# Kernel optimization log

Hardware: AMD Instinct MI355X
Metric: run time of the kernel (lower is better)

The kernel has to match this reference:

```python
import jax, jax.numpy as jnp
import numpy as np

B, S, INPUT_DIM = 8, 512, 64
D_MODEL, NUM_LAYERS, OUTPUT_DIM = 512, 4, 10
D_INNER, D_STATE, D_CONV, DT_RANK = 2 * D_MODEL, 16, 4, 32
GRID_SIZE, SPLINE_K = 5, 3
N_COEFF = GRID_SIZE + SPLINE_K  # 8
_H = 2.0 / GRID_SIZE
GRID = jnp.linspace(-1.0 - SPLINE_K * _H, 1.0 + SPLINE_K * _H, GRID_SIZE + 2 * SPLINE_K + 1)


def b_splines(x):
    # x: (..., in) -> (..., in, N_COEFF) via Cox-de Boor recursion on fixed GRID
    x = x[..., None]
    b = ((x >= GRID[:-1]) & (x < GRID[1:])).astype(x.dtype)
    for p in range(1, SPLINE_K + 1):
        left = (x - GRID[:-(p + 1)]) / (GRID[p:-1] - GRID[:-(p + 1)])
        right = (GRID[p + 1:] - x) / (GRID[p + 1:] - GRID[1:-p])
        b = left * b[..., :-1] + right * b[..., 1:]
    return b


def kan(x, base_w, spline_w):
    # efficient-KAN: silu base path + per-edge spline path
    return jax.nn.silu(x) @ base_w.T + jnp.einsum('...ik,oik->...o', b_splines(x), spline_w)


def layernorm(x, g, b):
    m = jnp.mean(x, -1, keepdims=True)
    v = jnp.var(x, -1, keepdims=True)
    return (x - m) / jnp.sqrt(v + 1e-5) * g + b


def liquid_proj(x, Win, Wrec, b, tau):
    # liquid time-constant RNN: h' = (tanh(Wx + Uh + b) - h) / tau
    pre = x @ Win  # (B,S,H)
    tau_pos = jax.nn.softplus(tau) + 0.1
    def step(h, p):
        act = jnp.tanh(p + h @ Wrec + b)
        h = h + (act - h) / tau_pos
        return h, h
    h0 = jnp.zeros((x.shape[0], Win.shape[1]), x.dtype)
    hT, hs = jax.lax.scan(step, h0, pre.transpose(1, 0, 2))
    return hs.transpose(1, 0, 2), hT


def mamba_block(x, in_proj_w, conv_w, conv_b, x_proj_w, dt_proj_w, dt_proj_b, A_log, Dp, out_proj_w):
    Bb, Ss, _ = x.shape
    xz = x @ in_proj_w.T                       # (B,S,2*di)
    xm, z = jnp.split(xz, 2, axis=-1)
    # causal depthwise conv1d with kernel D_CONV
    xp = jnp.pad(xm, ((0, 0), (D_CONV - 1, 0), (0, 0)))
    xm = sum(xp[:, k:k + Ss, :] * conv_w[:, k] for k in range(D_CONV)) + conv_b
    xm = jax.nn.silu(xm)
    x_dbl = xm @ x_proj_w.T                    # (B,S,dt_rank+2n)
    dt, Bc, Cc = jnp.split(x_dbl, [DT_RANK, DT_RANK + D_STATE], axis=-1)
    dt = jax.nn.softplus(dt @ dt_proj_w.T + dt_proj_b)   # (B,S,di)
    A = -jnp.exp(A_log)                        # (di,n)
    dA = jnp.exp(dt[..., None] * A)            # (B,S,di,n)
    dBu = dt[..., None] * Bc[:, :, None, :] * xm[..., None]
    def step(h, inp):
        a, bu, c = inp
        h = a * h + bu
        return h, jnp.einsum('bdn,bn->bd', h, c)
    h0 = jnp.zeros((Bb, D_INNER, D_STATE), x.dtype)
    _, ys = jax.lax.scan(step, h0, (dA.transpose(1, 0, 2, 3), dBu.transpose(1, 0, 2, 3), Cc.transpose(1, 0, 2)))
    y = ys.transpose(1, 0, 2) + Dp * xm
    y = y * jax.nn.silu(z)
    return y @ out_proj_w.T


def forward(x, lq_Win, lq_Wrec, lq_b, lq_tau, ln_g, ln_b, in_proj_w, conv_w, conv_b,
            x_proj_w, dt_proj_w, dt_proj_b, A_log, Dp, out_proj_w,
            kan_base_w, kan_spline_w, fn_g, fn_b, cls_base_w, cls_spline_w):
    x, _ = liquid_proj(x, lq_Win, lq_Wrec, lq_b, lq_tau)
    for l in range(NUM_LAYERS):
        residual = x
        xn = layernorm(x, ln_g[l], ln_b[l])
        xm = mamba_block(xn, in_proj_w[l], conv_w[l], conv_b[l], x_proj_w[l],
                         dt_proj_w[l], dt_proj_b[l], A_log[l], Dp[l], out_proj_w[l])
        x = residual + kan(xm, kan_base_w[l], kan_spline_w[l])
    x = layernorm(x, fn_g, fn_b)
    return kan(x.mean(axis=1), cls_base_w, cls_spline_w)


def setup_inputs():
    key = jax.random.key(0)
    ks = jax.random.split(key, 12)
    n = lambda k, shape, s: jax.random.normal(k, shape, jnp.float32) * s
    return {
        "x": n(ks[0], (B, S, INPUT_DIM), 1.0),
        "lq_Win": n(ks[1], (INPUT_DIM, D_MODEL), INPUT_DIM ** -0.5),
        "lq_Wrec": n(ks[2], (D_MODEL, D_MODEL), D_MODEL ** -0.5),
        "lq_b": jnp.zeros((D_MODEL,), jnp.float32),
        "lq_tau": jnp.ones((D_MODEL,), jnp.float32),
        "ln_g": jnp.ones((NUM_LAYERS, D_MODEL), jnp.float32),
        "ln_b": jnp.zeros((NUM_LAYERS, D_MODEL), jnp.float32),
        "in_proj_w": n(ks[3], (NUM_LAYERS, 2 * D_INNER, D_MODEL), D_MODEL ** -0.5),
        "conv_w": n(ks[4], (NUM_LAYERS, D_INNER, D_CONV), D_CONV ** -0.5),
        "conv_b": jnp.zeros((NUM_LAYERS, D_INNER), jnp.float32),
        "x_proj_w": n(ks[5], (NUM_LAYERS, DT_RANK + 2 * D_STATE, D_INNER), D_INNER ** -0.5),
        "dt_proj_w": n(ks[6], (NUM_LAYERS, D_INNER, DT_RANK), DT_RANK ** -0.5),
        "dt_proj_b": jnp.full((NUM_LAYERS, D_INNER), float(np.log(np.expm1(0.01))), jnp.float32),
        "A_log": jnp.log(jnp.broadcast_to(jnp.arange(1, D_STATE + 1, dtype=jnp.float32), (NUM_LAYERS, D_INNER, D_STATE))),
        "Dp": jnp.ones((NUM_LAYERS, D_INNER), jnp.float32),
        "out_proj_w": n(ks[7], (NUM_LAYERS, D_MODEL, D_INNER), D_INNER ** -0.5),
        "kan_base_w": n(ks[8], (NUM_LAYERS, D_MODEL, D_MODEL), D_MODEL ** -0.5),
        "kan_spline_w": n(ks[9], (NUM_LAYERS, D_MODEL, D_MODEL, N_COEFF), 0.1 * D_MODEL ** -0.5),
        "fn_g": jnp.ones((D_MODEL,), jnp.float32),
        "fn_b": jnp.zeros((D_MODEL,), jnp.float32),
        "cls_base_w": n(ks[10], (OUTPUT_DIM, D_MODEL), D_MODEL ** -0.5),
        "cls_spline_w": n(ks[11], (OUTPUT_DIM, D_MODEL, N_COEFF), 0.1 * D_MODEL ** -0.5),
    }


def reference(x, lq_Win, lq_Wrec, lq_b, lq_tau, ln_g, ln_b, in_proj_w, conv_w, conv_b,
              x_proj_w, dt_proj_w, dt_proj_b, A_log, Dp, out_proj_w,
              kan_base_w, kan_spline_w, fn_g, fn_b, cls_base_w, cls_spline_w):
    return forward(x, lq_Win, lq_Wrec, lq_b, lq_tau, ln_g, ln_b, in_proj_w, conv_w, conv_b,
                   x_proj_w, dt_proj_w, dt_proj_b, A_log, Dp, out_proj_w,
                   kan_base_w, kan_spline_w, fn_g, fn_b, cls_base_w, cls_spline_w)
```

## Files before the change

### kernel.cpp

```cpp
#include <hip/hip_runtime.h>
#include <hip/hip_bf16.h>
#include <cmath>

#define DEV __device__ __forceinline__

constexpr int B_ = 8, S_ = 512, IN_ = 64, D_ = 512, L_ = 4;
constexpr int DI_ = 1024, DCONV_ = 4, DTR_ = 32;
constexpr int ROWS = B_ * S_;

constexpr size_t MB = 1ull << 20;
constexpr size_t OFF_X    = 0;
constexpr size_t OFF_XN   = OFF_X   + 8*MB;
constexpr size_t OFF_XZ   = OFF_XN  + 8*MB;
constexpr size_t OFF_XM   = OFF_XZ  + 32*MB;
constexpr size_t OFF_DT   = OFF_XM  + 16*MB;
constexpr size_t OFF_XDBL = OFF_DT  + 16*MB;
constexpr size_t OFF_YG   = OFF_XDBL+ 1*MB;
constexpr size_t OFF_MO   = OFF_YG  + 16*MB;
constexpr size_t OFF_WINT = OFF_MO  + 8*MB;
constexpr size_t OFF_MEAN = OFF_WINT+ 128*1024;
constexpr size_t OFF_HBUF = OFF_MEAN+ 16*1024;
constexpr size_t OFF_FLG  = OFF_HBUF+ 32*1024;
constexpr size_t OFF_W16  = OFF_FLG + 64*1024;
constexpr size_t OFF_BASIS= OFF_XZ;

constexpr size_t W_IP = 0;
constexpr size_t W_OP = 1048576;
constexpr size_t W_KB = 1572864;
constexpr size_t W_KS = 1835008;
constexpr size_t W_XP = 3932160;
constexpr size_t W_DT = 3997696;
constexpr size_t W_PER_LAYER = 4030464;

DEV float siluf(float x){ return x / (1.f + __expf(-x)); }
DEV float softplusf(float x){ return fmaxf(x, 0.f) + log1pf(__expf(-fabsf(x))); }
DEV unsigned short f2h(float f){ return __builtin_bit_cast(unsigned short, (_Float16)f); }
DEV float h2f(unsigned short u){ return (float)__builtin_bit_cast(_Float16, u); }
DEV int pk2(float a, float b){ return (int)((unsigned)f2h(a) | ((unsigned)f2h(b) << 16)); }

typedef _Float16 half8 __attribute__((ext_vector_type(8)));
typedef float f32x4 __attribute__((ext_vector_type(4)));

DEV void bspline8(float x, float* bb){
  const float h = 0.4f, g0 = -2.2f;
  float b0[11];
#pragma unroll
  for (int j = 0; j < 11; ++j){
    float gj  = g0 + h * j;
    float gj1 = g0 + h * (j + 1);
    b0[j] = (x >= gj && x < gj1) ? 1.f : 0.f;
  }
#pragma unroll
  for (int p = 1; p <= 3; ++p){
    float inv = 1.f / (h * p);
#pragma unroll
    for (int j = 0; j + p < 11; ++j){
      float gj  = g0 + h * j;
      float gip = g0 + h * (j + p + 1);
      b0[j] = (x - gj) * inv * b0[j] + (gip - x) * inv * b0[j + 1];
    }
  }
#pragma unroll
  for (int c = 0; c < 8; ++c) bb[c] = b0[c];
}

__global__ __launch_bounds__(256)
void conv_w16(const float* __restrict__ ip, const float* __restrict__ op,
              const float* __restrict__ kb, const float* __restrict__ ks,
              const float* __restrict__ xp, const float* __restrict__ dt,
              unsigned short* __restrict__ w16)
{
  int blk = blockIdx.x, tid = threadIdx.x;
  const float* src; size_t doff; int sb;
  if      (blk < 512) { src = ip; doff = W_IP; sb = blk; }
  else if (blk < 768) { src = op; doff = W_OP; sb = blk - 512; }
  else if (blk < 896) { src = kb; doff = W_KB; sb = blk - 768; }
  else if (blk < 1920){ src = ks; doff = W_KS; sb = blk - 896; }
  else if (blk < 1952){ src = xp; doff = W_XP; sb = blk - 1920; }
  else                { src = dt; doff = W_DT; sb = blk - 1952; }
  size_t e = (size_t)sb * 2048 + tid * 8;
  float4 a = *(const float4*)(src + e), b = *(const float4*)(src + e + 4);
  int4 v = { pk2(a.x,a.y), pk2(a.z,a.w), pk2(b.x,b.y), pk2(b.z,b.w) };
  *(int4*)&w16[doff + e] = v;
}

template<bool SILU_A, int EPI>
__global__ __launch_bounds__(256)
void gemm_nt(const float* __restrict__ A, int lda,
             const float* __restrict__ W, int ldw,
             float* __restrict__ C, int ldc,
             const float* __restrict__ bias, int K)
{
  __shared__ float As[16][68];
  __shared__ float Ws[16][68];
  const int tid = threadIdx.x;
  const int m0 = blockIdx.y * 64, n0 = blockIdx.x * 64;
  const int lr = tid >> 2, lc = (tid & 3) * 4;
  const float* Ap = A + (size_t)(m0 + lr) * lda + lc;
  const float* Wp = W + (size_t)(n0 + lr) * ldw + lc;
  const int tx = tid & 15, ty = tid >> 4;
  float acc[4][4] = {};
  for (int k0 = 0; k0 < K; k0 += 16){
    float4 a = *(const float4*)(Ap + k0);
    float4 w = *(const float4*)(Wp + k0);
    if (SILU_A){ a.x = siluf(a.x); a.y = siluf(a.y); a.z = siluf(a.z); a.w = siluf(a.w); }
    __syncthreads();
    As[lc+0][lr] = a.x; As[lc+1][lr] = a.y; As[lc+2][lr] = a.z; As[lc+3][lr] = a.w;
    Ws[lc+0][lr] = w.x; Ws[lc+1][lr] = w.y; Ws[lc+2][lr] = w.z; Ws[lc+3][lr] = w.w;
    __syncthreads();
#pragma unroll
    for (int k = 0; k < 16; ++k){
      float4 av = *(const float4*)&As[k][ty*4];
      float4 wv = *(const float4*)&Ws[k][tx*4];
      acc[0][0] += av.x*wv.x; acc[0][1] += av.x*wv.y; acc[0][2] += av.x*wv.z; acc[0][3] += av.x*wv.w;
      acc[1][0] += av.y*wv.x; acc[1][1] += av.y*wv.y; acc[1][2] += av.y*wv.z; acc[1][3] += av.y*wv.w;
      acc[2][0] += av.z*wv.x; acc[2][1] += av.z*wv.y; acc[2][2] += av.z*wv.z; acc[2][3] += av.z*wv.w;
      acc[3][0] += av.w*wv.x; acc[3][1] += av.w*wv.y; acc[3][2] += av.w*wv.z; acc[3][3] += av.w*wv.w;
    }
  }
#pragma unroll
  for (int i = 0; i < 4; ++i){
    float* Crow = C + (size_t)(m0 + ty*4 + i) * ldc + n0 + tx*4;
    float4 r = {acc[i][0], acc[i][1], acc[i][2], acc[i][3]};
    *(float4*)Crow = r;
  }
}


template<int AMODE>
DEV void stage_a(const void* Av, int lda, int m0, int sr, int k0, int sh,
                 int4& av0, int4& av1)
{
  if (AMODE == 0){
    const unsigned short* ag = (const unsigned short*)Av + (size_t)(m0 + sr) * lda + k0 + sh*16;
    av0 = *(const int4*)ag; av1 = *(const int4*)(ag + 8);
  } else {
    const float* ag = (const float*)Av + (size_t)(m0 + sr) * lda + k0 + sh*16;
    float4 a0 = *(const float4*)ag,     a1 = *(const float4*)(ag+4);
    float4 a2 = *(const float4*)(ag+8), a3 = *(const float4*)(ag+12);
    if (AMODE == 2){
      a0.x=siluf(a0.x); a0.y=siluf(a0.y); a0.z=siluf(a0.z); a0.w=siluf(a0.w);
      a1.x=siluf(a1.x); a1.y=siluf(a1.y); a1.z=siluf(a1.z); a1.w=siluf(a1.w);
      a2.x=siluf(a2.x); a2.y=siluf(a2.y); a2.z=siluf(a2.z); a2.w=siluf(a2.w);
      a3.x=siluf(a3.x); a3.y=siluf(a3.y); a3.z=siluf(a3.z); a3.w=siluf(a3.w);
    }
    av0 = (int4){ pk2(a0.x,a0.y), pk2(a0.z,a0.w), pk2(a1.x,a1.y), pk2(a1.z,a1.w) };
    av1 = (int4){ pk2(a2.x,a2.y), pk2(a2.z,a2.w), pk2(a3.x,a3.y), pk2(a3.z,a3.w) };
  }
}

template<int EPI>
DEV void epi_store(void* Cv, size_t off, float v, const float* bias, int col)
{
  if (EPI == 0)      ((float*)Cv)[off] = v;
  else if (EPI == 1) ((float*)Cv)[off] += v;
  else if (EPI == 2) ((float*)Cv)[off] = softplusf(v + bias[col]);
  else               ((unsigned short*)Cv)[off] = f2h(v);
}

template<int AMODE, int EPI>
__global__ __launch_bounds__(256)
void gemm_h128(const void* __restrict__ Av, int lda,
               const unsigned short* __restrict__ W,
               void* __restrict__ Cv, int ldc,
               const float* __restrict__ bias, int K)
{
  __shared__ unsigned short As[128*40];
  __shared__ unsigned short Bs[128*40];
  const int tid = threadIdx.x;
  const int m0 = blockIdx.y * 128, n0 = blockIdx.x * 128;
  const int wid = tid >> 6, lane = tid & 63;
  const int wm = (wid & 1) * 64, wn = (wid >> 1) * 64;
  const int fr = lane & 15, fk = lane >> 4;
  const int sr = tid >> 1, sh = tid & 1;

  f32x4 acc[4][4];
#pragma unroll
  for (int i = 0; i < 4; ++i)
#pragma unroll
    for (int j = 0; j < 4; ++j)
#pragma unroll
      for (int r = 0; r < 4; ++r) acc[i][j][r] = 0.f;

  for (int k0 = 0; k0 < K; k0 += 32){
    int4 av0, av1;
    stage_a<AMODE>(Av, lda, m0, sr, k0, sh, av0, av1);
    const unsigned short* wg = W + (size_t)(n0 + sr) * K + k0 + sh*16;
    int4 bv0 = *(const int4*)wg, bv1 = *(const int4*)(wg + 8);
    __syncthreads();
    *(int4*)&As[sr*40 + sh*16]     = av0;
    *(int4*)&As[sr*40 + sh*16 + 8] = av1;
    *(int4*)&Bs[sr*40 + sh*16]     = bv0;
    *(int4*)&Bs[sr*40 + sh*16 + 8] = bv1;
    __syncthreads();
    half8 a[4], b[4];
#pragma unroll
    for (int i = 0; i < 4; ++i) a[i] = *(const half8*)&As[(wm + i*16 + fr)*40 + fk*8];
#pragma unroll
    for (int j = 0; j < 4; ++j) b[j] = *(const half8*)&Bs[(wn + j*16 + fr)*40 + fk*8];
#pragma unroll
    for (int i = 0; i < 4; ++i)
#pragma unroll
      for (int j = 0; j < 4; ++j)
        acc[i][j] = __builtin_amdgcn_mfma_f32_16x16x32_f16(a[i], b[j], acc[i][j], 0, 0, 0);
  }
#pragma unroll
  for (int i = 0; i < 4; ++i)
#pragma unroll
    for (int j = 0; j < 4; ++j){
      int col = n0 + wn + j*16 + fr;
#pragma unroll
      for (int r = 0; r < 4; ++r){
        int row = m0 + wm + i*16 + fk*4 + r;
        epi_store<EPI>(Cv, (size_t)row * ldc + col, acc[i][j][r], bias, col);
      }
    }
}

template<int AMODE, int EPI>
__global__ __launch_bounds__(256)
void gemm_h64(const void* __restrict__ Av, int lda,
              const unsigned short* __restrict__ W,
              void* __restrict__ Cv, int ldc,
              const float* __restrict__ bias, int K)
{
  __shared__ unsigned short As[128*40];
  __shared__ unsigned short Bs[64*40];
  const int tid = threadIdx.x;
  const int m0 = blockIdx.y * 128, n0 = blockIdx.x * 64;
  const int wid = tid >> 6, lane = tid & 63;
  const int fr = lane & 15, fk = lane >> 4;
  const int sr = tid >> 1, sh = tid & 1;
  const int br = tid >> 2, bq = tid & 3;

  f32x4 acc[2][4];
#pragma unroll
  for (int i = 0; i < 2; ++i)
#pragma unroll
    for (int j = 0; j < 4; ++j)
#pragma unroll
      for (int r = 0; r < 4; ++r) acc[i][j][r] = 0.f;

  for (int k0 = 0; k0 < K; k0 += 32){
    int4 av0, av1;
    stage_a<AMODE>(Av, lda, m0, sr, k0, sh, av0, av1);
    const unsigned short* wg = W + (size_t)(n0 + br) * K + k0 + bq*8;
    int4 bv0 = *(const int4*)wg;
    __syncthreads();
    *(int4*)&As[sr*40 + sh*16]     = av0;
    *(int4*)&As[sr*40 + sh*16 + 8] = av1;
    *(int4*)&Bs[br*40 + bq*8]      = bv0;
    __syncthreads();
    half8 a[2], b[4];
#pragma unroll
    for (int i = 0; i < 2; ++i) a[i] = *(const half8*)&As[(wid*32 + i*16 + fr)*40 + fk*8];
#pragma unroll
    for (int j = 0; j < 4; ++j) b[j] = *(const half8*)&Bs[(j*16 + fr)*40 + fk*8];
#pragma unroll
    for (int i = 0; i < 2; ++i)
#pragma unroll
      for (int j = 0; j < 4; ++j)
        acc[i][j] = __builtin_amdgcn_mfma_f32_16x16x32_f16(a[i], b[j], acc[i][j], 0, 0, 0);
  }
#pragma unroll
  for (int i = 0; i < 2; ++i)
#pragma unroll
    for (int j = 0; j < 4; ++j){
      int col = n0 + j*16 + fr;
#pragma unroll
      for (int r = 0; r < 4; ++r){
        int row = m0 + wid*32 + i*16 + fk*4 + r;
        epi_store<EPI>(Cv, (size_t)row * ldc + col, acc[i][j][r], bias, col);
      }
    }
}

__global__ __launch_bounds__(256)
void transpose_win(const float* __restrict__ Win, float* __restrict__ WinT)
{
  int idx = blockIdx.x * 256 + threadIdx.x;
  int n = idx >> 6, k = idx & 63;
  WinT[idx] = Win[(size_t)k * 512 + n];
}

__global__ __launch_bounds__(512)
void liquid_scan3(const float* __restrict__ pre, const float* __restrict__ Wrec,
                  const float* __restrict__ bias, const float* __restrict__ tau,
                  float* __restrict__ xout, float* __restrict__ hbuf,
                  unsigned* __restrict__ flags)
{
  __shared__ float Wl[32800];
  __shared__ float hl[544];
  __shared__ float hnew[64];
  const int tid = threadIdx.x;
  const int bid = blockIdx.x;
  const int slice = bid >> 3, b = bid & 7;
  for (int idx = tid; idx < 512*16; idx += 512){
    int k = idx >> 4, c4 = (idx & 15) * 4;
    float4 w = *(const float4*)(Wrec + (size_t)k*512 + slice*64 + c4);
    *(float4*)&Wl[k*64 + c4 + (k>>6)*4] = w;
  }
  hl[tid + (tid>>6)*4] = 0.f;
  const int o = tid >> 3, kl = tid & 7;
  const int og = slice*64 + o;
  const float tauinv = 1.f / (softplusf(tau[og]) + 0.1f);
  const float bo = bias[og];
  float hold = 0.f;
  const float* preb = pre + (size_t)b * S_ * 512;
  float* xb = xout + (size_t)b * S_ * 512;
  float* hb0 = hbuf + (size_t)b * 512;
  unsigned* bflags = flags + b*8*16;
  unsigned* myflag = bflags + slice*16;
  const int kbase = kl * 64;
  const float* wp = &Wl[(size_t)kbase*64 + o + kl*4];
  __syncthreads();
  for (int t = 0; t < S_; ++t){
    float prev = (kl == 0) ? preb[(size_t)t*512 + og] : 0.f;
    float hreg[64];
#pragma unroll
    for (int j4 = 0; j4 < 16; ++j4)
      *(float4*)&hreg[j4*4] = *(const float4*)&hl[kbase + kl*4 + j4*4];
    float s = 0.f;
#pragma unroll
    for (int j = 0; j < 64; ++j)
      s += hreg[j] * wp[(size_t)j * 64];
    s += __shfl_xor(s, 1);
    s += __shfl_xor(s, 2);
    s += __shfl_xor(s, 4);
    if (kl == 0){
      float act = tanhf(s + prev + bo);
      hold += (act - hold) * tauinv;
      xb[(size_t)t*512 + og] = hold;
      hnew[o] = hold;
    }
    __syncthreads();
    if (tid < 64)
      __hip_atomic_store(hb0 + (t&1)*4096 + slice*64 + tid, hnew[tid],
                         __ATOMIC_RELAXED, __HIP_MEMORY_SCOPE_AGENT);
    if (tid == 0){
      asm volatile("s_waitcnt vmcnt(0)" ::: "memory");
      __hip_atomic_store(myflag, (unsigned)(t+1),
                         __ATOMIC_RELAXED, __HIP_MEMORY_SCOPE_AGENT);
    }
    if (tid < 8){
      while (__hip_atomic_load(bflags + tid*16, __ATOMIC_RELAXED,
                               __HIP_MEMORY_SCOPE_AGENT) < (unsigned)(t+1)) { }
    }
    __syncthreads();
    float hv = __hip_atomic_load(hb0 + (t&1)*4096 + tid,
                                 __ATOMIC_RELAXED, __HIP_MEMORY_SCOPE_AGENT);
    hl[tid + (tid>>6)*4] = hv;
    __syncthreads();
  }
}

__global__ __launch_bounds__(256)
void conv_silu(const unsigned short* __restrict__ xz, const float* __restrict__ cw,
               const float* __restrict__ cb, unsigned short* __restrict__ xm)
{
  int idx = blockIdx.x * 256 + threadIdx.x;
  int d = idx & 1023;
  int bs = idx >> 10;
  int t = bs & 511;
  const unsigned short* p = xz + (size_t)bs * 2048 + d;
  float4 w = *(const float4*)(cw + d*4);
  float acc = cb[d] + w.w * h2f(p[0]);
  if (t >= 1) acc += w.z * h2f(p[-2048]);
  if (t >= 2) acc += w.y * h2f(p[-2*2048]);
  if (t >= 3) acc += w.x * h2f(p[-3*2048]);
  xm[idx] = f2h(siluf(acc));
}

__global__ __launch_bounds__(256)
void mamba_scan2(const float* __restrict__ dt, const unsigned short* __restrict__ xm,
                 const float* __restrict__ xdbl, const unsigned short* __restrict__ xz,
                 const float* __restrict__ A_log, const float* __restrict__ Dp,
                 unsigned short* __restrict__ yg)
{
  const int tid = threadIdx.x;
  const int wave = tid >> 6, lane = tid & 63;
  const int ch = lane >> 3, sub = lane & 7;
  const int d = blockIdx.x * 32 + wave * 8 + ch;
  const int b = blockIdx.y;
  float2 al = *(const float2*)(A_log + (size_t)d*16 + sub*2);
  const float A0 = -__expf(al.x), A1 = -__expf(al.y);
  const float Dv = Dp[d];
  float h0 = 0.f, h1 = 0.f;
  const size_t rb = (size_t)b * S_;
  const float* dtp = dt + rb*1024 + d;
  const unsigned short* xmp = xm + rb*1024 + d;
  const unsigned short* zp  = xz + rb*2048 + 1024 + d;
  const float* bcp = xdbl + rb*64 + 32 + sub*2;
  const float* ccp = xdbl + rb*64 + 48 + sub*2;
  unsigned short* yp = yg + rb*1024 + d;
#pragma unroll 2
  for (int t = 0; t < S_; ++t){
    float dtv = dtp[(size_t)t*1024];
    float xv  = h2f(xmp[(size_t)t*1024]);
    float2 B2 = *(const float2*)(bcp + (size_t)t*64);
    float2 C2 = *(const float2*)(ccp + (size_t)t*64);
    float cbu = dtv * xv;
    h0 = __expf(dtv * A0) * h0 + cbu * B2.x;
    h1 = __expf(dtv * A1) * h1 + cbu * B2.y;
    float y = h0 * C2.x + h1 * C2.y;
    y += __shfl_xor(y, 1);
    y += __shfl_xor(y, 2);
    y += __shfl_xor(y, 4);
    if (sub == 0){
      float zv = h2f(zp[(size_t)t*2048]);
      yp[(size_t)t*1024] = f2h((y + Dv * xv) * siluf(zv));
    }
  }
}

template<bool H>
__global__ __launch_bounds__(256)
void layernorm_k(const float* __restrict__ x, const float* __restrict__ g,
                 const float* __restrict__ b, void* __restrict__ y)
{
  __shared__ float red[8];
  const int row = blockIdx.x, tid = threadIdx.x;
  const float* xr = x + (size_t)row * 512;
  float2 v = *(const float2*)(xr + tid*2);
  float s = v.x + v.y;
#pragma unroll
  for (int o = 32; o; o >>= 1) s += __shfl_xor(s, o);
  if ((tid & 63) == 0) red[tid >> 6] = s;
  __syncthreads();
  float mean = (red[0] + red[1] + red[2] + red[3]) * (1.f/512.f);
  float dx = v.x - mean, dy = v.y - mean;
  float q = dx*dx + dy*dy;
#pragma unroll
  for (int o = 32; o; o >>= 1) q += __shfl_xor(q, o);
  if ((tid & 63) == 0) red[4 + (tid >> 6)] = q;
  __syncthreads();
  float var = (red[4] + red[5] + red[6] + red[7]) * (1.f/512.f);
  float rstd = rsqrtf(var + 1e-5f);
  float2 gg = *(const float2*)(g + tid*2);
  float2 bb = *(const float2*)(b + tid*2);
  float ox = dx*rstd*gg.x + bb.x;
  float oy = dy*rstd*gg.y + bb.y;
  if (H){
    unsigned* yr = (unsigned*)y + (size_t)row*256 + tid;
    *yr = (unsigned)f2h(ox) | ((unsigned)f2h(oy) << 16);
  } else {
    float2 o2 = {ox, oy};
    *(float2*)((float*)y + (size_t)row*512 + tid*2) = o2;
  }
}

__global__ __launch_bounds__(256)
void bspline_kernel(const float* __restrict__ xin, unsigned short* __restrict__ basis)
{
  int idx = blockIdx.x * 256 + threadIdx.x;
  float x = xin[idx];
  float bb[8];
  bspline8(x, bb);
  int4 v = { pk2(bb[0],bb[1]), pk2(bb[2],bb[3]), pk2(bb[4],bb[5]), pk2(bb[6],bb[7]) };
  *(int4*)(basis + (size_t)idx * 8) = v;
}

__global__ __launch_bounds__(512)
void mean_over_s(const float* __restrict__ x, float* __restrict__ out)
{
  int b = blockIdx.x, d = threadIdx.x;
  const float* p = x + (size_t)b*S_*512 + d;
  float s = 0.f;
  for (int t = 0; t < S_; ++t) s += p[(size_t)t*512];
  out[b*512 + d] = s * (1.f/512.f);
}

__global__ __launch_bounds__(64)
void cls_kan(const float* __restrict__ xmean, const float* __restrict__ bw,
             const float* __restrict__ sw, float* __restrict__ out)
{
  int o = blockIdx.x % 10, b = blockIdx.x / 10;
  int lane = threadIdx.x;
  float acc = 0.f;
  for (int i = lane; i < 512; i += 64){
    float xv = xmean[b*512 + i];
    acc += siluf(xv) * bw[o*512 + i];
    float bb[8]; bspline8(xv, bb);
    const float* sp = sw + ((size_t)(o*512 + i)) * 8;
#pragma unroll
    for (int c = 0; c < 8; ++c) acc += bb[c] * sp[c];
  }
#pragma unroll
  for (int off = 32; off; off >>= 1) acc += __shfl_xor(acc, off);
  if (lane == 0) out[b*10 + o] = acc;
}

extern "C" void kernel_launch(void* const* d_in, const int* in_sizes, int n_in,
                              void* d_out, int out_size, void* d_ws, size_t ws_size,
                              hipStream_t stream)
{
  const float* x_in    = (const float*)d_in[0];
  const float* lq_Win  = (const float*)d_in[1];
  const float* lq_Wrec = (const float*)d_in[2];
  const float* lq_b    = (const float*)d_in[3];
  const float* lq_tau  = (const float*)d_in[4];
  const float* ln_g    = (const float*)d_in[5];
  const float* ln_bi   = (const float*)d_in[6];
  const float* in_proj = (const float*)d_in[7];
  const float* conv_w  = (const float*)d_in[8];
  const float* conv_b  = (const float*)d_in[9];
  const float* x_proj  = (const float*)d_in[10];
  const float* dt_w    = (const float*)d_in[11];
  const float* dt_b    = (const float*)d_in[12];
  const float* A_log   = (const float*)d_in[13];
  const float* Dp      = (const float*)d_in[14];
  const float* out_w   = (const float*)d_in[15];
  const float* kb_w    = (const float*)d_in[16];
  const float* ks_w    = (const float*)d_in[17];
  const float* fn_g    = (const float*)d_in[18];
  const float* fn_b    = (const float*)d_in[19];
  const float* cb_w    = (const float*)d_in[20];
  const float* cs_w    = (const float*)d_in[21];
  float* out = (float*)d_out;

  char* ws = (char*)d_ws;
  float* xcur  = (float*)(ws + OFF_X);
  float* xn32  = (float*)(ws + OFF_XN);
  unsigned short* xn16 = (unsigned short*)(ws + OFF_XN);
  unsigned short* xz16 = (unsigned short*)(ws + OFF_XZ);
  unsigned short* xm16 = (unsigned short*)(ws + OFF_XM);
  float* dtb   = (float*)(ws + OFF_DT);
  float* xdbl  = (float*)(ws + OFF_XDBL);
  unsigned short* yg16 = (unsigned short*)(ws + OFF_YG);
  float* mo    = (float*)(ws + OFF_MO);
  float* wint  = (float*)(ws + OFF_WINT);
  float* xmean = (float*)(ws + OFF_MEAN);
  float* hbufp = (float*)(ws + OFF_HBUF);
  unsigned* flgp = (unsigned*)(ws + OFF_FLG);
  unsigned short* w16 = (unsigned short*)(ws + OFF_W16);
  unsigned short* basis = (unsigned short*)(ws + OFF_BASIS);

  transpose_win<<<128, 256, 0, stream>>>(lq_Win, wint);
  gemm_nt<false,0><<<dim3(D_/64, ROWS/64), 256, 0, stream>>>(x_in, IN_, wint, IN_, xn32, D_, nullptr, IN_);
  hipMemsetAsync(flgp, 0, 8*8*16*sizeof(unsigned), stream);
  liquid_scan3<<<64, 512, 0, stream>>>(xn32, lq_Wrec, lq_b, lq_tau, xcur, hbufp, flgp);

  for (int l = 0; l < L_; ++l){
    conv_w16<<<1968, 256, 0, stream>>>(
        in_proj + (size_t)l*2*DI_*D_, out_w + (size_t)l*D_*DI_,
        kb_w + (size_t)l*D_*D_, ks_w + (size_t)l*D_*D_*8,
        x_proj + (size_t)l*64*DI_, dt_w + (size_t)l*DI_*DTR_,
        w16 + (size_t)l*W_PER_LAYER);
  }

  for (int l = 0; l < L_; ++l){
    const unsigned short* wl = w16 + (size_t)l*W_PER_LAYER;
    layernorm_k<true><<<ROWS, 256, 0, stream>>>(xcur, ln_g + l*D_, ln_bi + l*D_, xn16);
    gemm_h128<0,3><<<dim3(16, 32), 256, 0, stream>>>(
        xn16, D_, wl + W_IP, xz16, 2*DI_, nullptr, D_);
    conv_silu<<<ROWS*DI_/256, 256, 0, stream>>>(xz16, conv_w + l*DI_*DCONV_, conv_b + l*DI_, xm16);
    gemm_h64<0,0><<<dim3(1, 32), 256, 0, stream>>>(
        xm16, DI_, wl + W_XP, xdbl, 64, nullptr, DI_);
    gemm_h64<1,2><<<dim3(16, 32), 256, 0, stream>>>(
        xdbl, 64, wl + W_DT, dtb, DI_, dt_b + l*DI_, DTR_);
    mamba_scan2<<<dim3(32, 8), 256, 0, stream>>>(
        dtb, xm16, xdbl, xz16, A_log + (size_t)l*DI_*16, Dp + l*DI_, yg16);
    gemm_h64<0,0><<<dim3(8, 32), 256, 0, stream>>>(
        yg16, DI_, wl + W_OP, mo, D_, nullptr, DI_);
    bspline_kernel<<<ROWS*D_/256, 256, 0, stream>>>(mo, basis);
    gemm_h64<2,1><<<dim3(8, 32), 256, 0, stream>>>(
        mo, D_, wl + W_KB, xcur, D_, nullptr, D_);
    gemm_h64<0,1><<<dim3(8, 32), 256, 0, stream>>>(
        basis, D_*8, wl + W_KS, xcur, D_, nullptr, D_*8);
  }

  layernorm_k<false><<<ROWS, 256, 0, stream>>>(xcur, fn_g, fn_b, xn32);
  mean_over_s<<<B_, 512, 0, stream>>>(xn32, xmean);
  cls_kan<<<B_*10, 64, 0, stream>>>(xmean, cb_w, cs_w, out);
}
```

Before: 3.789 ms.

## Fuse x_proj with dt_proj, merge KAN GEMMs, store dt in half precision

Fuses the x_proj GEMM with the dt_proj GEMM plus softplus in a single kernel that keeps the x_dbl tile in shared memory, and writes dt as fp16 instead of fp32 to halve scan input traffic. Merges the KAN base and spline GEMMs into one kernel that accumulates both into registers and does a single read-modify-write of the residual. Moves the liquid-scan output store after the barrier so it is off the critical inter-block handoff. Risks include lower dt precision and lower parallelism in the fused xproj kernel, which launches only 32 blocks.

```diff
diff --git a/kernel.cpp b/kernel.cpp
--- a/kernel.cpp
+++ b/kernel.cpp
@@ -150,11 +150,10 @@
 }
 
 template<int EPI>
-DEV void epi_store(void* Cv, size_t off, float v, const float* bias, int col)
+DEV void epi_store(void* Cv, size_t off, float v)
 {
   if (EPI == 0)      ((float*)Cv)[off] = v;
   else if (EPI == 1) ((float*)Cv)[off] += v;
-  else if (EPI == 2) ((float*)Cv)[off] = softplusf(v + bias[col]);
   else               ((unsigned short*)Cv)[off] = f2h(v);
 }
 
@@ -162,8 +161,7 @@
 __global__ __launch_bounds__(256)
 void gemm_h128(const void* __restrict__ Av, int lda,
                const unsigned short* __restrict__ W,
-               void* __restrict__ Cv, int ldc,
-               const float* __restrict__ bias, int K)
+               void* __restrict__ Cv, int ldc, int K)
 {
   __shared__ unsigned short As[128*40];
   __shared__ unsigned short Bs[128*40];
@@ -212,7 +210,7 @@
 #pragma unroll
       for (int r = 0; r < 4; ++r){
         int row = m0 + wm + i*16 + fk*4 + r;
-        epi_store<EPI>(Cv, (size_t)row * ldc + col, acc[i][j][r], bias, col);
+        epi_store<EPI>(Cv, (size_t)row * ldc + col, acc[i][j][r]);
       }
     }
 }
@@ -221,8 +219,7 @@
 __global__ __launch_bounds__(256)
 void gemm_h64(const void* __restrict__ Av, int lda,
               const unsigned short* __restrict__ W,
-              void* __restrict__ Cv, int ldc,
-              const float* __restrict__ bias, int K)
+              void* __restrict__ Cv, int ldc, int K)
 {
   __shared__ unsigned short As[128*40];
   __shared__ unsigned short Bs[64*40];
@@ -270,7 +267,164 @@
 #pragma unroll
       for (int r = 0; r < 4; ++r){
         int row = m0 + wid*32 + i*16 + fk*4 + r;
-        epi_store<EPI>(Cv, (size_t)row * ldc + col, acc[i][j][r], bias, col);
+        epi_store<EPI>(Cv, (size_t)row * ldc + col, acc[i][j][r]);
+      }
+    }
+}
+
+__global__ __launch_bounds__(256)
+void xproj_dt(const unsigned short* __restrict__ xm,
+              const unsigned short* __restrict__ wxp,
+              const unsigned short* __restrict__ wdt,
+              const float* __restrict__ dtb,
+              float* __restrict__ xdbl, unsigned short* __restrict__ dt16)
+{
+  __shared__ unsigned short As[128*40];
+  __shared__ unsigned short Bs[64*40];
+  __shared__ unsigned short Xl[128*72];
+  const int tid = threadIdx.x;
+  const int m0 = blockIdx.x * 128;
+  const int wid = tid >> 6, lane = tid & 63;
+  const int fr = lane & 15, fk = lane >> 4;
+  const int sr = tid >> 1, sh = tid & 1;
+  const int br = tid >> 2, bq = tid & 3;
+
+  f32x4 acc[2][4];
+#pragma unroll
+  for (int i = 0; i < 2; ++i)
+#pragma unroll
+    for (int j = 0; j < 4; ++j)
+#pragma unroll
+      for (int r = 0; r < 4; ++r) acc[i][j][r] = 0.f;
+
+  for (int k0 = 0; k0 < 1024; k0 += 32){
+    const unsigned short* ag = xm + (size_t)(m0 + sr) * 1024 + k0 + sh*16;
+    int4 av0 = *(const int4*)ag, av1 = *(const int4*)(ag + 8);
+    const unsigned short* wg = wxp + (size_t)br * 1024 + k0 + bq*8;
+    int4 bv0 = *(const int4*)wg;
+    __syncthreads();
+    *(int4*)&As[sr*40 + sh*16]     = av0;
+    *(int4*)&As[sr*40 + sh*16 + 8] = av1;
+    *(int4*)&Bs[br*40 + bq*8]      = bv0;
+    __syncthreads();
+    half8 a[2], b[4];
+#pragma unroll
+    for (int i = 0; i < 2; ++i) a[i] = *(const half8*)&As[(wid*32 + i*16 + fr)*40 + fk*8];
+#pragma unroll
+    for (int j = 0; j < 4; ++j) b[j] = *(const half8*)&Bs[(j*16 + fr)*40 + fk*8];
+#pragma unroll
+    for (int i = 0; i < 2; ++i)
+#pragma unroll
+      for (int j = 0; j < 4; ++j)
+        acc[i][j] = __builtin_amdgcn_mfma_f32_16x16x32_f16(a[i], b[j], acc[i][j], 0, 0, 0);
+  }
+#pragma unroll
+  for (int i = 0; i < 2; ++i)
+#pragma unroll
+    for (int j = 0; j < 4; ++j){
+      int col = j*16 + fr;
+#pragma unroll
+      for (int r = 0; r < 4; ++r){
+        int row = wid*32 + i*16 + fk*4 + r;
+        float v = acc[i][j][r];
+        xdbl[(size_t)(m0 + row) * 64 + col] = v;
+        Xl[row*72 + col] = f2h(v);
+      }
+    }
+  __syncthreads();
+  half8 a2[2];
+#pragma unroll
+  for (int i = 0; i < 2; ++i) a2[i] = *(const half8*)&Xl[(wid*32 + i*16 + fr)*72 + fk*8];
+  for (int j = 0; j < 64; ++j){
+    half8 b = *(const half8*)&wdt[(size_t)(j*16 + fr)*32 + fk*8];
+    f32x4 c0 = {0.f,0.f,0.f,0.f}, c1 = {0.f,0.f,0.f,0.f};
+    c0 = __builtin_amdgcn_mfma_f32_16x16x32_f16(a2[0], b, c0, 0, 0, 0);
+    c1 = __builtin_amdgcn_mfma_f32_16x16x32_f16(a2[1], b, c1, 0, 0, 0);
+    int col = j*16 + fr;
+    float bias = dtb[col];
+#pragma unroll
+    for (int r = 0; r < 4; ++r){
+      int row0 = wid*32 + fk*4 + r;
+      int row1 = row0 + 16;
+      dt16[(size_t)(m0 + row0) * 1024 + col] = f2h(softplusf(c0[r] + bias));
+      dt16[(size_t)(m0 + row1) * 1024 + col] = f2h(softplusf(c1[r] + bias));
+    }
+  }
+}
+
+__global__ __launch_bounds__(256)
+void gemm_kan(const float* __restrict__ mo, const unsigned short* __restrict__ basis,
+              const unsigned short* __restrict__ wkb, const unsigned short* __restrict__ wks,
+              float* __restrict__ xcur)
+{
+  __shared__ unsigned short As[128*40];
+  __shared__ unsigned short Bs[64*40];
+  const int tid = threadIdx.x;
+  const int m0 = blockIdx.y * 128, n0 = blockIdx.x * 64;
+  const int wid = tid >> 6, lane = tid & 63;
+  const int fr = lane & 15, fk = lane >> 4;
+  const int sr = tid >> 1, sh = tid & 1;
+  const int br = tid >> 2, bq = tid & 3;
+
+  f32x4 acc[2][4];
+#pragma unroll
+  for (int i = 0; i < 2; ++i)
+#pragma unroll
+    for (int j = 0; j < 4; ++j)
+#pragma unroll
+      for (int r = 0; r < 4; ++r) acc[i][j][r] = 0.f;
+
+  for (int k0 = 0; k0 < 512; k0 += 32){
+    int4 av0, av1;
+    stage_a<2>(mo, 512, m0, sr, k0, sh, av0, av1);
+    const unsigned short* wg = wkb + (size_t)(n0 + br) * 512 + k0 + bq*8;
+    int4 bv0 = *(const int4*)wg;
+    __syncthreads();
+    *(int4*)&As[sr*40 + sh*16]     = av0;
+    *(int4*)&As[sr*40 + sh*16 + 8] = av1;
+    *(int4*)&Bs[br*40 + bq*8]      = bv0;
+    __syncthreads();
+    half8 a[2], b[4];
+#pragma unroll
+    for (int i = 0; i < 2; ++i) a[i] = *(const half8*)&As[(wid*32 + i*16 + fr)*40 + fk*8];
+#pragma unroll
+    for (int j = 0; j < 4; ++j) b[j] = *(const half8*)&Bs[(j*16 + fr)*40 + fk*8];
+#pragma unroll
+    for (int i = 0; i < 2; ++i)
+#pragma unroll
+      for (int j = 0; j < 4; ++j)
+        acc[i][j] = __builtin_amdgcn_mfma_f32_16x16x32_f16(a[i], b[j], acc[i][j], 0, 0, 0);
+  }
+  for (int k0 = 0; k0 < 4096; k0 += 32){
+    int4 av0, av1;
+    stage_a<0>(basis, 4096, m0, sr, k0, sh, av0, av1);
+    const unsigned short* wg = wks + (size_t)(n0 + br) * 4096 + k0 + bq*8;
+    int4 bv0 = *(const int4*)wg;
+    __syncthreads();
+    *(int4*)&As[sr*40 + sh*16]     = av0;
+    *(int4*)&As[sr*40 + sh*16 + 8] = av1;
+    *(int4*)&Bs[br*40 + bq*8]      = bv0;
+    __syncthreads();
+    half8 a[2], b[4];
+#pragma unroll
+    for (int i = 0; i < 2; ++i) a[i] = *(const half8*)&As[(wid*32 + i*16 + fr)*40 + fk*8];
+#pragma unroll
+    for (int j = 0; j < 4; ++j) b[j] = *(const half8*)&Bs[(j*16 + fr)*40 + fk*8];
+#pragma unroll
+    for (int i = 0; i < 2; ++i)
+#pragma unroll
+      for (int j = 0; j < 4; ++j)
+        acc[i][j] = __builtin_amdgcn_mfma_f32_16x16x32_f16(a[i], b[j], acc[i][j], 0, 0, 0);
+  }
+#pragma unroll
+  for (int i = 0; i < 2; ++i)
+#pragma unroll
+    for (int j = 0; j < 4; ++j){
+      int col = n0 + j*16 + fr;
+#pragma unroll
+      for (int r = 0; r < 4; ++r){
+        int row = m0 + wid*32 + i*16 + fk*4 + r;
+        xcur[(size_t)row * 512 + col] += acc[i][j][r];
       }
     }
 }
@@ -330,7 +484,6 @@
     if (kl == 0){
       float act = tanhf(s + prev + bo);
       hold += (act - hold) * tauinv;
-      xb[(size_t)t*512 + og] = hold;
       hnew[o] = hold;
     }
     __syncthreads();
@@ -347,6 +500,8 @@
                                __HIP_MEMORY_SCOPE_AGENT) < (unsigned)(t+1)) { }
     }
     __syncthreads();
+    if (kl == 0)
+      xb[(size_t)t*512 + og] = hold;
     float hv = __hip_atomic_load(hb0 + (t&1)*4096 + tid,
                                  __ATOMIC_RELAXED, __HIP_MEMORY_SCOPE_AGENT);
     hl[tid + (tid>>6)*4] = hv;
@@ -372,7 +527,7 @@
 }
 
 __global__ __launch_bounds__(256)
-void mamba_scan2(const float* __restrict__ dt, const unsigned short* __restrict__ xm,
+void mamba_scan2(const unsigned short* __restrict__ dt, const unsigned short* __restrict__ xm,
                  const float* __restrict__ xdbl, const unsigned short* __restrict__ xz,
                  const float* __restrict__ A_log, const float* __restrict__ Dp,
                  unsigned short* __restrict__ yg)
@@ -387,7 +542,7 @@
   const float Dv = Dp[d];
   float h0 = 0.f, h1 = 0.f;
   const size_t rb = (size_t)b * S_;
-  const float* dtp = dt + rb*1024 + d;
+  const unsigned short* dtp = dt + rb*1024 + d;
   const unsigned short* xmp = xm + rb*1024 + d;
   const unsigned short* zp  = xz + rb*2048 + 1024 + d;
   const float* bcp = xdbl + rb*64 + 32 + sub*2;
@@ -395,7 +550,7 @@
   unsigned short* yp = yg + rb*1024 + d;
 #pragma unroll 2
   for (int t = 0; t < S_; ++t){
-    float dtv = dtp[(size_t)t*1024];
+    float dtv = h2f(dtp[(size_t)t*1024]);
     float xv  = h2f(xmp[(size_t)t*1024]);
     float2 B2 = *(const float2*)(bcp + (size_t)t*64);
     float2 C2 = *(const float2*)(ccp + (size_t)t*64);
@@ -524,7 +679,7 @@
   unsigned short* xn16 = (unsigned short*)(ws + OFF_XN);
   unsigned short* xz16 = (unsigned short*)(ws + OFF_XZ);
   unsigned short* xm16 = (unsigned short*)(ws + OFF_XM);
-  float* dtb   = (float*)(ws + OFF_DT);
+  unsigned short* dt16 = (unsigned short*)(ws + OFF_DT);
   float* xdbl  = (float*)(ws + OFF_XDBL);
   unsigned short* yg16 = (unsigned short*)(ws + OFF_YG);
   float* mo    = (float*)(ws + OFF_MO);
@@ -552,21 +707,17 @@
     const unsigned short* wl = w16 + (size_t)l*W_PER_LAYER;
     layernorm_k<true><<<ROWS, 256, 0, stream>>>(xcur, ln_g + l*D_, ln_bi + l*D_, xn16);
     gemm_h128<0,3><<<dim3(16, 32), 256, 0, stream>>>(
-        xn16, D_, wl + W_IP, xz16, 2*DI_, nullptr, D_);
+        xn16, D_, wl + W_IP, xz16, 2*DI_, D_);
     conv_silu<<<ROWS*DI_/256, 256, 0, stream>>>(xz16, conv_w + l*DI_*DCONV_, conv_b + l*DI_, xm16);
-    gemm_h64<0,0><<<dim3(1, 32), 256, 0, stream>>>(
-        xm16, DI_, wl + W_XP, xdbl, 64, nullptr, DI_);
-    gemm_h64<1,2><<<dim3(16, 32), 256, 0, stream>>>(
-        xdbl, 64, wl + W_DT, dtb, DI_, dt_b + l*DI_, DTR_);
+    xproj_dt<<<32, 256, 0, stream>>>(
+        xm16, wl + W_XP, wl + W_DT, dt_b + l*DI_, xdbl, dt16);
     mamba_scan2<<<dim3(32, 8), 256, 0, stream>>>(
-        dtb, xm16, xdbl, xz16, A_log + (size_t)l*DI_*16, Dp + l*DI_, yg16);
+        dt16, xm16, xdbl, xz16, A_log + (size_t)l*DI_*16, Dp + l*DI_, yg16);
     gemm_h64<0,0><<<dim3(8, 32), 256, 0, stream>>>(
-        yg16, DI_, wl + W_OP, mo, D_, nullptr, DI_);
+        yg16, DI_, wl + W_OP, mo, D_, DI_);
     bspline_kernel<<<ROWS*D_/256, 256, 0, stream>>>(mo, basis);
-    gemm_h64<2,1><<<dim3(8, 32), 256, 0, stream>>>(
-        mo, D_, wl + W_KB, xcur, D_, nullptr, D_);
-    gemm_h64<0,1><<<dim3(8, 32), 256, 0, stream>>>(
-        basis, D_*8, wl + W_KS, xcur, D_, nullptr, D_*8);
+    gemm_kan<<<dim3(8, 32), 256, 0, stream>>>(
+        mo, basis, wl + W_KB, wl + W_KS, xcur);
   }
 
   layernorm_k<false><<<ROWS, 256, 0, stream>>>(xcur, fn_g, fn_b, xn32);
```

Result: slower. 4.220 ms (+11.4%).
